# Performance work log

Hardware: AMD Instinct MI355X
Metric: run time of the kernel (lower is better)

The kernel has to match this reference:

```python
import jax, jax.numpy as jnp
import numpy as np

DIM = 384
NUM_HEADS = 12
DILATIONS = (1, 2, 3)
KSZ = 3
B, N = 4, 8192
HEAD_DIM = DIM // NUM_HEADS          # 32
ND = len(DILATIONS)                  # num_dilation
CD = DIM // ND                       # channels per dilation group
SCALE = HEAD_DIM ** -0.5


def setup_inputs() -> dict:
    key = jax.random.key(0)
    k0, k1, k2 = jax.random.split(key, 3)
    s = 0.02
    return {
        "x": jax.random.normal(k0, (B, N, DIM), dtype=jnp.float32),
        "Wqkv": jax.random.normal(k1, (3 * DIM, DIM), dtype=jnp.float32) * s,
        "bqkv": jnp.zeros((3 * DIM,), dtype=jnp.float32),
        "Wproj": jax.random.normal(k2, (DIM, DIM), dtype=jnp.float32) * s,
        "bproj": jnp.zeros((DIM,), dtype=jnp.float32),
    }


def _unfold_seq(t, dil, ksz):
    # Faithful nn.Unfold(ksz, dilation=dil, padding=dil*(ksz-1)//2) applied to
    # t viewed as (B, C, N, 1): of the ksz*ksz taps, only the center-width
    # column is in-bounds; the rest are zero padding. Tap order is (kh, kw)
    # with kw fastest, matching torch's unfold channel layout.
    # t: (B, nh, hd, N) -> (B, nh, hd, ksz*ksz, N)
    _, _, _, n = t.shape
    pad = dil * (ksz - 1) // 2
    tp = jnp.pad(t, ((0, 0), (0, 0), (0, 0), (pad, pad)))
    zeros = jnp.zeros_like(t)
    taps = []
    for kh in range(ksz):
        row = jax.lax.dynamic_slice_in_dim(tp, kh * dil, n, axis=3)
        for kw in range(ksz):
            taps.append(row if kw == ksz // 2 else zeros)
    return jnp.stack(taps, axis=3)


def _dilate_attn(q, k, v, dil):
    # q,k,v: (B, CD, N) -> (B, N, CD)
    b, cd, n = q.shape
    nh = cd // HEAD_DIM
    q = q.reshape(b, nh, HEAD_DIM, n)
    k = _unfold_seq(k.reshape(b, nh, HEAD_DIM, n), dil, KSZ)   # (b,nh,hd,k2,n)
    v = _unfold_seq(v.reshape(b, nh, HEAD_DIM, n), dil, KSZ)
    attn = jax.nn.softmax(jnp.einsum("bhdn,bhdjn->bhnj", q, k) * SCALE, axis=-1)
    out = jnp.einsum("bhnj,bhdjn->bhnd", attn, v)              # (b,nh,n,hd)
    return out.transpose(0, 2, 1, 3).reshape(b, n, cd)


def reference(x, Wqkv, bqkv, Wproj, bproj):
    b, n, c = x.shape
    # (b,n,3c) -> (nd, 3, b, cd, n), matching torch permute(3,2,0,4,1)
    qkv = (x @ Wqkv.T + bqkv).reshape(b, n, 3, ND, CD).transpose(3, 2, 0, 4, 1)
    outs = [_dilate_attn(qkv[i, 0], qkv[i, 1], qkv[i, 2], DILATIONS[i]) for i in range(ND)]
    xo = jnp.stack(outs, axis=2).reshape(b, n, c)  # (b,n,nd,cd) -> (b,n,c)
    return xo @ Wproj.T + bproj
```

## Files before the change

### kernel.cpp

```cpp
#include <hip/hip_runtime.h>

#define DIM     384
#define QKV_CH  1152
#define HD      32
#define CD      128
#define BATCH   4
#define SEQ     8192
#define ROWS    (BATCH*SEQ)
#define SCALE   0.17677669529663687f

typedef short bf16x8 __attribute__((ext_vector_type(8)));
typedef float f32x4  __attribute__((ext_vector_type(4)));

__device__ __forceinline__ unsigned short f2bf(float f) {
  unsigned int u = __float_as_uint(f);
  u += 0x7fffu + ((u >> 16) & 1u);
  return (unsigned short)(u >> 16);
}
__device__ __forceinline__ float bf2f(unsigned short b) {
  return __uint_as_float(((unsigned int)b) << 16);
}
__device__ __forceinline__ void unpack8(uint4 u, float* f) {
  f[0] = bf2f((unsigned short)(u.x & 0xffffu)); f[1] = bf2f((unsigned short)(u.x >> 16));
  f[2] = bf2f((unsigned short)(u.y & 0xffffu)); f[3] = bf2f((unsigned short)(u.y >> 16));
  f[4] = bf2f((unsigned short)(u.z & 0xffffu)); f[5] = bf2f((unsigned short)(u.z >> 16));
  f[6] = bf2f((unsigned short)(u.w & 0xffffu)); f[7] = bf2f((unsigned short)(u.w >> 16));
}

__global__ __launch_bounds__(256) void cvt_f32_bf16(const float* __restrict__ in,
                                                    unsigned short* __restrict__ out,
                                                    int n4) {
  int i = blockIdx.x * 256 + threadIdx.x;
  if (i >= n4) return;
  float4 v = ((const float4*)in)[i];
  ushort4 o;
  o.x = f2bf(v.x); o.y = f2bf(v.y); o.z = f2bf(v.z); o.w = f2bf(v.w);
  ((ushort4*)out)[i] = o;
}

template<int OUT_BF16>
__global__ __launch_bounds__(256) void gemm_bt(const unsigned short* __restrict__ A,
                                               const unsigned short* __restrict__ Bt,
                                               const float* __restrict__ bias,
                                               void* __restrict__ Cv,
                                               int M, int Nt, int K) {
  __shared__ unsigned short As[128 * 32];
  __shared__ unsigned short Bs[128 * 32];
  const int t = threadIdx.x;
  const int wave = t >> 6, lane = t & 63;
  const int quad = lane >> 4, l16 = lane & 15;
  const int row0 = blockIdx.x * 128, col0 = blockIdx.y * 128;
  const int wm = (wave & 1) * 64, wn = (wave >> 1) * 64;

  f32x4 acc[4][4] = {};

  for (int k0 = 0; k0 < K; k0 += 32) {
#pragma unroll
    for (int r = 0; r < 2; ++r) {
      int c  = r * 256 + t;
      int rr = c >> 2, cc = (c & 3) * 8;
      *(uint4*)&As[rr * 32 + cc] = *(const uint4*)&A [(size_t)(row0 + rr) * K + k0 + cc];
      *(uint4*)&Bs[rr * 32 + cc] = *(const uint4*)&Bt[(size_t)(col0 + rr) * K + k0 + cc];
    }
    __syncthreads();

    bf16x8 af[4], bfv[4];
#pragma unroll
    for (int mi = 0; mi < 4; ++mi)
      af[mi] = *(bf16x8*)&As[(wm + mi * 16 + l16) * 32 + quad * 8];
#pragma unroll
    for (int ni = 0; ni < 4; ++ni)
      bfv[ni] = *(bf16x8*)&Bs[(wn + ni * 16 + l16) * 32 + quad * 8];
#pragma unroll
    for (int mi = 0; mi < 4; ++mi)
#pragma unroll
      for (int ni = 0; ni < 4; ++ni)
        acc[mi][ni] = __builtin_amdgcn_mfma_f32_16x16x32_bf16(af[mi], bfv[ni], acc[mi][ni], 0, 0, 0);
    __syncthreads();
  }

#pragma unroll
  for (int mi = 0; mi < 4; ++mi) {
#pragma unroll
    for (int ni = 0; ni < 4; ++ni) {
      int gc = col0 + wn + ni * 16 + l16;
      float bv = bias[gc];
#pragma unroll
      for (int r = 0; r < 4; ++r) {
        int gr = row0 + wm + mi * 16 + quad * 4 + r;
        float val = acc[mi][ni][r] + bv;
        if (OUT_BF16) ((unsigned short*)Cv)[(size_t)gr * Nt + gc] = f2bf(val);
        else          ((float*)Cv)[(size_t)gr * Nt + gc] = val;
      }
    }
  }
}

__global__ __launch_bounds__(256) void attn_kernel(const unsigned short* __restrict__ qkv,
                                                   unsigned short* __restrict__ out) {
  int tid = blockIdx.x * 256 + threadIdx.x;
  int i  = tid / 12;
  int dh = tid - i * 12;
  int d = dh >> 2, h = dh & 3;
  int dil = d + 1;
  int n = i & (SEQ - 1);
  size_t base = (size_t)i * QKV_CH + d * CD + h * HD;

  float q[32];
  {
    const uint4* qp = (const uint4*)(qkv + base);
#pragma unroll
    for (int c = 0; c < 4; ++c) unpack8(qp[c], &q[c * 8]);
  }

  float ex[3];
  int   valid[3];
#pragma unroll
  for (int kh = 0; kh < 3; ++kh) {
    int off = (kh - 1) * dil;
    int nn = n + off;
    int v = (nn >= 0) && (nn < SEQ);
    valid[kh] = v;
    float l = 0.f;
    if (v) {
      const uint4* kp = (const uint4*)(qkv + base + DIM + (ptrdiff_t)off * QKV_CH);
#pragma unroll
      for (int c = 0; c < 4; ++c) {
        float kk[8]; unpack8(kp[c], kk);
#pragma unroll
        for (int j = 0; j < 8; ++j) l += q[c * 8 + j] * kk[j];
      }
    }
    ex[kh] = __expf(l * SCALE);
  }
  float inv = 1.f / (ex[0] + ex[1] + ex[2] + 6.f);

  float o[32];
#pragma unroll
  for (int e = 0; e < 32; ++e) o[e] = 0.f;
#pragma unroll
  for (int kh = 0; kh < 3; ++kh) {
    if (!valid[kh]) continue;
    int off = (kh - 1) * dil;
    const uint4* vp = (const uint4*)(qkv + base + 2 * DIM + (ptrdiff_t)off * QKV_CH);
    float w = ex[kh];
#pragma unroll
    for (int c = 0; c < 4; ++c) {
      float vv[8]; unpack8(vp[c], vv);
#pragma unroll
      for (int j = 0; j < 8; ++j) o[c * 8 + j] += w * vv[j];
    }
  }

  unsigned short* op = out + (size_t)i * DIM + d * CD + h * HD;
#pragma unroll
  for (int c = 0; c < 4; ++c) {
    unsigned int w0 = (unsigned int)f2bf(o[c*8+0] * inv) | ((unsigned int)f2bf(o[c*8+1] * inv) << 16);
    unsigned int w1 = (unsigned int)f2bf(o[c*8+2] * inv) | ((unsigned int)f2bf(o[c*8+3] * inv) << 16);
    unsigned int w2 = (unsigned int)f2bf(o[c*8+4] * inv) | ((unsigned int)f2bf(o[c*8+5] * inv) << 16);
    unsigned int w3 = (unsigned int)f2bf(o[c*8+6] * inv) | ((unsigned int)f2bf(o[c*8+7] * inv) << 16);
    uint4 u; u.x = w0; u.y = w1; u.z = w2; u.w = w3;
    ((uint4*)op)[c] = u;
  }
}

extern "C" void kernel_launch(void* const* d_in, const int* in_sizes, int n_in,
                              void* d_out, int out_size, void* d_ws, size_t ws_size,
                              hipStream_t stream) {
  const float* x     = (const float*)d_in[0];
  const float* Wqkv  = (const float*)d_in[1];
  const float* bqkv  = (const float*)d_in[2];
  const float* Wproj = (const float*)d_in[3];
  const float* bproj = (const float*)d_in[4];
  float* out = (float*)d_out;

  char* ws = (char*)d_ws;
  unsigned short* qkv_bf   = (unsigned short*)(ws);
  unsigned short* x_bf     = (unsigned short*)(ws + 75497472);
  unsigned short* attn_bf  = (unsigned short*)(ws + 100663296);
  unsigned short* wqkv_bf  = (unsigned short*)(ws + 125829120);
  unsigned short* wproj_bf = (unsigned short*)(ws + 126713856);

  cvt_f32_bf16<<<(ROWS * DIM / 4) / 256, 256, 0, stream>>>(x, x_bf, ROWS * DIM / 4);
  cvt_f32_bf16<<<(QKV_CH * DIM / 4 + 255) / 256, 256, 0, stream>>>(Wqkv, wqkv_bf, QKV_CH * DIM / 4);
  cvt_f32_bf16<<<(DIM * DIM / 4 + 255) / 256, 256, 0, stream>>>(Wproj, wproj_bf, DIM * DIM / 4);

  gemm_bt<1><<<dim3(ROWS / 128, QKV_CH / 128), 256, 0, stream>>>(
      x_bf, wqkv_bf, bqkv, (void*)qkv_bf, ROWS, QKV_CH, DIM);

  attn_kernel<<<(ROWS * 12) / 256, 256, 0, stream>>>(qkv_bf, attn_bf);

  gemm_bt<0><<<dim3(ROWS / 128, DIM / 128), 256, 0, stream>>>(
      attn_bf, wproj_bf, bproj, (void*)out, ROWS, DIM, DIM);
}
```

Baseline: 200.1 us.

## Use direct global-to-LDS loads and transposed MFMA for vectorized GEMM epilogue

The GEMM now stages A and B tiles with the global_load_lds builtin, bypassing registers, and makes K and the output width compile-time constants so the K loop fully unrolls. Swapping the MFMA operands transposes the accumulator layout, so each lane holds four consecutive columns. The epilogue can then load bias as float4 and write packed uint2/float4 stores instead of scattered scalar writes. The LDS destination indexing relies on the per-lane contiguous layout of global_load_lds, which carries correctness risk if that mapping does not match the tile layout.

```diff
diff --git a/kernel.cpp b/kernel.cpp
--- a/kernel.cpp
+++ b/kernel.cpp
@@ -38,12 +38,11 @@
   ((ushort4*)out)[i] = o;
 }
 
-template<int OUT_BF16>
+template<int OUT_BF16, int K, int NT>
 __global__ __launch_bounds__(256) void gemm_bt(const unsigned short* __restrict__ A,
                                                const unsigned short* __restrict__ Bt,
                                                const float* __restrict__ bias,
-                                               void* __restrict__ Cv,
-                                               int M, int Nt, int K) {
+                                               void* __restrict__ Cv) {
   __shared__ unsigned short As[128 * 32];
   __shared__ unsigned short Bs[128 * 32];
   const int t = threadIdx.x;
@@ -54,13 +53,18 @@
 
   f32x4 acc[4][4] = {};
 
+#pragma unroll
   for (int k0 = 0; k0 < K; k0 += 32) {
 #pragma unroll
     for (int r = 0; r < 2; ++r) {
       int c  = r * 256 + t;
       int rr = c >> 2, cc = (c & 3) * 8;
-      *(uint4*)&As[rr * 32 + cc] = *(const uint4*)&A [(size_t)(row0 + rr) * K + k0 + cc];
-      *(uint4*)&Bs[rr * 32 + cc] = *(const uint4*)&Bt[(size_t)(col0 + rr) * K + k0 + cc];
+      __builtin_amdgcn_global_load_lds(
+          (const __attribute__((address_space(1))) void*)&A[(size_t)(row0 + rr) * K + k0 + cc],
+          (__attribute__((address_space(3))) void*)&As[8 * c], 16, 0, 0);
+      __builtin_amdgcn_global_load_lds(
+          (const __attribute__((address_space(1))) void*)&Bt[(size_t)(col0 + rr) * K + k0 + cc],
+          (__attribute__((address_space(3))) void*)&Bs[8 * c], 16, 0, 0);
     }
     __syncthreads();
 
@@ -75,22 +79,33 @@
     for (int mi = 0; mi < 4; ++mi)
 #pragma unroll
       for (int ni = 0; ni < 4; ++ni)
-        acc[mi][ni] = __builtin_amdgcn_mfma_f32_16x16x32_bf16(af[mi], bfv[ni], acc[mi][ni], 0, 0, 0);
+        acc[mi][ni] = __builtin_amdgcn_mfma_f32_16x16x32_bf16(bfv[ni], af[mi], acc[mi][ni], 0, 0, 0);
     __syncthreads();
   }
 
+  float4 bv[4];
+#pragma unroll
+  for (int ni = 0; ni < 4; ++ni)
+    bv[ni] = *(const float4*)&bias[col0 + wn + ni * 16 + quad * 4];
+
 #pragma unroll
   for (int mi = 0; mi < 4; ++mi) {
+    size_t gr = (size_t)(row0 + wm + mi * 16 + l16);
 #pragma unroll
     for (int ni = 0; ni < 4; ++ni) {
-      int gc = col0 + wn + ni * 16 + l16;
-      float bv = bias[gc];
-#pragma unroll
-      for (int r = 0; r < 4; ++r) {
-        int gr = row0 + wm + mi * 16 + quad * 4 + r;
-        float val = acc[mi][ni][r] + bv;
-        if (OUT_BF16) ((unsigned short*)Cv)[(size_t)gr * Nt + gc] = f2bf(val);
-        else          ((float*)Cv)[(size_t)gr * Nt + gc] = val;
+      int gc = col0 + wn + ni * 16 + quad * 4;
+      float v0 = acc[mi][ni][0] + bv[ni].x;
+      float v1 = acc[mi][ni][1] + bv[ni].y;
+      float v2 = acc[mi][ni][2] + bv[ni].z;
+      float v3 = acc[mi][ni][3] + bv[ni].w;
+      if (OUT_BF16) {
+        uint2 u;
+        u.x = (unsigned int)f2bf(v0) | ((unsigned int)f2bf(v1) << 16);
+        u.y = (unsigned int)f2bf(v2) | ((unsigned int)f2bf(v3) << 16);
+        *(uint2*)&((unsigned short*)Cv)[gr * NT + gc] = u;
+      } else {
+        float4 o; o.x = v0; o.y = v1; o.z = v2; o.w = v3;
+        *(float4*)&((float*)Cv)[gr * NT + gc] = o;
       }
     }
   }
@@ -185,11 +200,11 @@
   cvt_f32_bf16<<<(QKV_CH * DIM / 4 + 255) / 256, 256, 0, stream>>>(Wqkv, wqkv_bf, QKV_CH * DIM / 4);
   cvt_f32_bf16<<<(DIM * DIM / 4 + 255) / 256, 256, 0, stream>>>(Wproj, wproj_bf, DIM * DIM / 4);
 
-  gemm_bt<1><<<dim3(ROWS / 128, QKV_CH / 128), 256, 0, stream>>>(
-      x_bf, wqkv_bf, bqkv, (void*)qkv_bf, ROWS, QKV_CH, DIM);
+  gemm_bt<1, DIM, QKV_CH><<<dim3(ROWS / 128, QKV_CH / 128), 256, 0, stream>>>(
+      x_bf, wqkv_bf, bqkv, (void*)qkv_bf);
 
   attn_kernel<<<(ROWS * 12) / 256, 256, 0, stream>>>(qkv_bf, attn_bf);
 
-  gemm_bt<0><<<dim3(ROWS / 128, DIM / 128), 256, 0, stream>>>(
-      attn_bf, wproj_bf, bproj, (void*)out, ROWS, DIM, DIM);
-}
+  gemm_bt<0, DIM, DIM><<<dim3(ROWS / 128, DIM / 128), 256, 0, stream>>>(
+      attn_bf, wproj_bf, bproj, (void*)out);
+}
```

Measured after the change: 206.9 us. 1.03x slower.
